# Kernel optimization log

Measured on AMD Instinct MI355X. Metric: run time of the kernel, lower is better.

## Reference

```python
import jax, jax.numpy as jnp
import numpy as np

N_NODES = 100000
N_EDGES = 1600000
IN_DIM, HID, OUT = 128, 64, 64
KERNEL = 5
PAD = (KERNEL - 1) // 2


def setup_inputs() -> dict:
    key = jax.random.key(0)
    ks = jax.random.split(key, 12)
    s = lambda fan_in: 1.0 / np.sqrt(fan_in)
    return {
        "x": jax.random.normal(ks[0], (N_NODES, IN_DIM), jnp.float32),
        "edge_index": jax.random.randint(ks[1], (2, N_EDGES), 0, N_NODES, jnp.int32),
        "W0": jax.random.normal(ks[2], (IN_DIM, HID), jnp.float32) * s(IN_DIM),
        "b0": jnp.zeros((HID,), jnp.float32),
        "W1": jax.random.normal(ks[3], (HID, HID), jnp.float32) * s(HID),
        "b1": jnp.zeros((HID,), jnp.float32),
        "W2": jax.random.normal(ks[4], (HID, OUT), jnp.float32) * s(HID),
        "b2": jnp.zeros((OUT,), jnp.float32),
        "Wp": jax.random.normal(ks[5], (OUT, 1), jnp.float32) * s(OUT),
        "bp": jnp.zeros((1,), jnp.float32),
        "conv1_w": jax.random.normal(ks[6], (OUT, OUT, KERNEL), jnp.float32) * s(OUT * KERNEL),
        "conv1_b": jnp.zeros((OUT,), jnp.float32),
        "conv2_w": jax.random.normal(ks[7], (OUT, OUT, KERNEL), jnp.float32) * s(OUT * KERNEL),
        "conv2_b": jnp.zeros((OUT,), jnp.float32),
        "lin_w": jax.random.normal(ks[8], (2 * OUT, OUT), jnp.float32) * s(2 * OUT),
        "lin_b": jnp.zeros((OUT,), jnp.float32),
    }


def gcn_conv(h, W, b, src, dst, n):
    """PyG GCNConv: x @ W, add self-loops, D^-1/2 (A+I) D^-1/2 aggregation, + bias."""
    h = h @ W  # [N, out]
    loop = jnp.arange(n, dtype=src.dtype)
    srcl = jnp.concatenate([src, loop])
    dstl = jnp.concatenate([dst, loop])
    deg = jax.ops.segment_sum(jnp.ones_like(dstl, dtype=h.dtype), dstl, num_segments=n)
    dinv = jnp.where(deg > 0, jax.lax.rsqrt(deg), 0.0)
    norm = dinv[srcl] * dinv[dstl]  # [E+N]
    out = jax.ops.segment_sum(h[srcl] * norm[:, None], dstl, num_segments=n)
    return out + b


def conv1d(x, w, b):
    # x: [1, C, N], w: [Cout, Cin, K]
    y = jax.lax.conv_general_dilated(x, w, window_strides=(1,), padding=[(PAD, PAD)],
                                     dimension_numbers=("NCH", "OIH", "NCH"))
    return y + b[None, :, None]


def reference(x, edge_index, W0, b0, W1, b1, W2, b2, Wp, bp,
              conv1_w, conv1_b, conv2_w, conv2_b, lin_w, lin_b):
    n = x.shape[0]
    src, dst = edge_index[0], edge_index[1]
    # eval mode: dropout layers are identity
    h = jax.nn.relu(gcn_conv(x, W0, b0, src, dst, n))
    h = jax.nn.relu(gcn_conv(h, W1, b1, src, dst, n))
    h1 = gcn_conv(h, W2, b2, src, dst, n)  # [N, OUT]
    g_score = h1 @ Wp + bp  # [N, 1]
    sorted_idx = jnp.argsort(g_score[:, 0])  # ascending, as torch.sort
    inverse_idx = jnp.argsort(sorted_idx)
    sorted_x = g_score[sorted_idx] * h1[sorted_idx]  # [N, OUT]
    sorted_x = sorted_x.T[None]  # [1, OUT, N]
    sorted_x = jax.nn.relu(conv1d(sorted_x, conv1_w, conv1_b))
    sorted_x = conv1d(sorted_x, conv2_w, conv2_b)
    sorted_x = sorted_x[0].T  # [N, OUT]
    h2 = sorted_x[inverse_idx]  # un-sort back to node order
    out = jnp.concatenate([h1, h2], axis=1) @ lin_w + lin_b  # [N, OUT]
    return out
```

## Files before the change

### kernel.cpp

```cpp
#include <hip/hip_runtime.h>

#define NN 100000
#define NE 1600000
#define NBUK 391
#define RBLK 98
#define NENT (256 * RBLK)
#define RSEG 25
#define BS_CHUNK 8192
#define NBS 196

__global__ void zero_bhist(int* bhist) {
    int i = blockIdx.x * blockDim.x + threadIdx.x;
    if (i < NBUK) bhist[i] = 0;
}

__global__ __launch_bounds__(256) void bucket_hist(const int* __restrict__ dst, int* __restrict__ bhist) {
    __shared__ int h[NBUK];
    int t = threadIdx.x;
    for (int b = t; b < NBUK; b += 256) h[b] = 0;
    __syncthreads();
    int base = blockIdx.x * BS_CHUNK;
    for (int i = t; i < BS_CHUNK; i += 256) {
        int e = base + i;
        if (e < NE) atomicAdd(&h[dst[e] >> 8], 1);
    }
    __syncthreads();
    for (int b = t; b < NBUK; b += 256)
        if (h[b]) atomicAdd(&bhist[b], h[b]);
}

__global__ __launch_bounds__(512) void bucket_scan(const int* __restrict__ bhist,
                                                   int* __restrict__ bbase, int* __restrict__ bcur) {
    __shared__ int tmp[512];
    int t = threadIdx.x;
    int v = (t < NBUK) ? bhist[t] : 0;
    tmp[t] = v; __syncthreads();
    for (int o = 1; o < 512; o <<= 1) {
        int add = (t >= o) ? tmp[t - o] : 0;
        __syncthreads();
        tmp[t] += add;
        __syncthreads();
    }
    int ex = tmp[t] - v;
    if (t < NBUK) { bbase[t] = ex; bcur[t] = ex; }
    if (t == NBUK - 1) bbase[NBUK] = ex + v;
}

__global__ __launch_bounds__(256) void bucket_scatter(const int* __restrict__ src,
                                                      const int* __restrict__ dst,
                                                      int* __restrict__ bcur,
                                                      unsigned* __restrict__ stage) {
    __shared__ int h[NBUK];
    int t = threadIdx.x;
    for (int b = t; b < NBUK; b += 256) h[b] = 0;
    __syncthreads();
    int base = blockIdx.x * BS_CHUNK;
    for (int i = t; i < BS_CHUNK; i += 256) {
        int e = base + i;
        if (e < NE) atomicAdd(&h[dst[e] >> 8], 1);
    }
    __syncthreads();
    for (int b = t; b < NBUK; b += 256) {
        int c = h[b];
        h[b] = c ? atomicAdd(&bcur[b], c) : 0;
    }
    __syncthreads();
    for (int i = t; i < BS_CHUNK; i += 256) {
        int e = base + i;
        if (e < NE) {
            int d = dst[e];
            int p = atomicAdd(&h[d >> 8], 1);
            stage[p] = ((unsigned)src[e] << 8) | (unsigned)(d & 255);
        }
    }
}

__global__ __launch_bounds__(256) void csr_place(const unsigned* __restrict__ stage,
                                                 const int* __restrict__ bbase,
                                                 int* __restrict__ csr,
                                                 int* __restrict__ counts,
                                                 int* __restrict__ offs,
                                                 float* __restrict__ dinv) {
    __shared__ int cnt[256];
    __shared__ int cursor[256];
    int b = blockIdx.x, t = threadIdx.x;
    int start = bbase[b], end = bbase[b + 1];
    cnt[t] = 0;
    __syncthreads();
    for (int idx = start + t; idx < end; idx += 256)
        atomicAdd(&cnt[stage[idx] & 255u], 1);
    __syncthreads();
    int c = cnt[t];
    __shared__ int tmp[256];
    tmp[t] = c; __syncthreads();
    for (int o = 1; o < 256; o <<= 1) {
        int add = (t >= o) ? tmp[t - o] : 0;
        __syncthreads();
        tmp[t] += add;
        __syncthreads();
    }
    int pos = start + tmp[t] - c;
    cursor[t] = pos;
    int node = b * 256 + t;
    if (node < NN) {
        offs[node] = pos;
        counts[node] = c;
        dinv[node] = rsqrtf((float)(c + 1));
    }
    __syncthreads();
    for (int idx = start + t; idx < end; idx += 256) {
        unsigned u = stage[idx];
        int p = atomicAdd(&cursor[u & 255u], 1);
        csr[p] = (int)(u >> 8);
    }
}

__device__ inline void swz_w(const float* __restrict__ W, float4* __restrict__ o, int idx) {
    int k4 = idx >> 6, co = idx & 63;
    o[idx] = make_float4(W[(4 * k4 + 0) * 64 + co], W[(4 * k4 + 1) * 64 + co],
                         W[(4 * k4 + 2) * 64 + co], W[(4 * k4 + 3) * 64 + co]);
}

__device__ inline void swz_c(const float* __restrict__ w, float4* __restrict__ o, int idx) {
    int co = idx & 63, j = (idx >> 6) & 15, k = idx >> 10;
    int b = co * 320 + k;
    o[idx] = make_float4(w[b + (4 * j + 0) * 5], w[b + (4 * j + 1) * 5],
                         w[b + (4 * j + 2) * 5], w[b + (4 * j + 3) * 5]);
}

__global__ void swizzle_all(const float* W0, const float* W1, const float* W2,
                            const float* lw, const float* c1w, const float* c2w,
                            float4* w0sw, float4* w1sw, float4* w2sw,
                            float4* linsw, float4* c1sw, float4* c2sw) {
    int idx = blockIdx.x * blockDim.x + threadIdx.x;
    if (idx < 2048)        swz_w(W0, w0sw, idx);
    else if (idx < 3072)   swz_w(W1, w1sw, idx - 2048);
    else if (idx < 4096)   swz_w(W2, w2sw, idx - 3072);
    else if (idx < 6144)   swz_w(lw, linsw, idx - 4096);
    else if (idx < 11264)  swz_c(c1w, c1sw, idx - 6144);
    else if (idx < 16384)  swz_c(c2w, c2sw, idx - 11264);
}

template <int K, bool RELU>
__global__ __launch_bounds__(256) void gemm64r(const float* __restrict__ X,
                                               const float4* __restrict__ Wsw,
                                               const float* __restrict__ dinv,
                                               float* __restrict__ Y, int n) {
    constexpr int KV = K / 4;
    constexpr int SH = (KV == 32) ? 5 : 4;
    __shared__ float4 xs[64][KV];
    int tid = threadIdx.x;
    int r0 = blockIdx.x * 64;
    for (int idx = tid; idx < 64 * KV; idx += 256) {
        int r = idx >> SH, k4 = idx & (KV - 1);
        int row = r0 + r;
        float4 v = make_float4(0.f, 0.f, 0.f, 0.f);
        if (row < n) v = *reinterpret_cast<const float4*>(X + (size_t)row * K + 4 * k4);
        if (RELU) {
            v.x = fmaxf(v.x, 0.f); v.y = fmaxf(v.y, 0.f);
            v.z = fmaxf(v.z, 0.f); v.w = fmaxf(v.w, 0.f);
        }
        xs[r][k4] = v;
    }
    __syncthreads();
    int co2 = tid & 31, rg = tid >> 5;
    int c0 = 2 * co2;
    float acc0[8], acc1[8];
#pragma unroll
    for (int i = 0; i < 8; i++) { acc0[i] = 0.f; acc1[i] = 0.f; }
    for (int k4 = 0; k4 < KV; k4++) {
        float4 wa = Wsw[k4 * 64 + c0];
        float4 wb = Wsw[k4 * 64 + c0 + 1];
#pragma unroll
        for (int i = 0; i < 8; i++) {
            float4 xv = xs[rg * 8 + i][k4];
            acc0[i] += xv.x * wa.x + xv.y * wa.y + xv.z * wa.z + xv.w * wa.w;
            acc1[i] += xv.x * wb.x + xv.y * wb.y + xv.z * wb.z + xv.w * wb.w;
        }
    }
#pragma unroll
    for (int i = 0; i < 8; i++) {
        int row = r0 + rg * 8 + i;
        if (row < n) {
            float dv = dinv[row];
            *reinterpret_cast<float2*>(Y + (size_t)row * 64 + c0) =
                make_float2(acc0[i] * dv, acc1[i] * dv);
        }
    }
}

template <int SCORE>
__global__ __launch_bounds__(256) void agg_pull(const float* __restrict__ H,
                                                const int* __restrict__ offs,
                                                const int* __restrict__ counts,
                                                const int* __restrict__ csr,
                                                const float* __restrict__ dinv,
                                                const float* __restrict__ bias,
                                                float* __restrict__ Y,
                                                const float* __restrict__ Wp,
                                                const float* __restrict__ bp,
                                                float* __restrict__ sc,
                                                unsigned* __restrict__ keys,
                                                int* __restrict__ vals) {
    int lane = threadIdx.x & 63;
    int node = blockIdx.x * 4 + (threadIdx.x >> 6);
    if (node >= NN) return;
    float dv = dinv[node];
    float acc = H[(size_t)node * 64 + lane];
    int off = offs[node], cnt = counts[node];
    int i = 0;
    for (; i + 7 < cnt; i += 8) {
        int p0 = csr[off + i];
        int p1 = csr[off + i + 1];
        int p2 = csr[off + i + 2];
        int p3 = csr[off + i + 3];
        int p4 = csr[off + i + 4];
        int p5 = csr[off + i + 5];
        int p6 = csr[off + i + 6];
        int p7 = csr[off + i + 7];
        float h0 = H[(size_t)p0 * 64 + lane];
        float h1 = H[(size_t)p1 * 64 + lane];
        float h2 = H[(size_t)p2 * 64 + lane];
        float h3 = H[(size_t)p3 * 64 + lane];
        float h4 = H[(size_t)p4 * 64 + lane];
        float h5 = H[(size_t)p5 * 64 + lane];
        float h6 = H[(size_t)p6 * 64 + lane];
        float h7 = H[(size_t)p7 * 64 + lane];
        acc += ((h0 + h1) + (h2 + h3)) + ((h4 + h5) + (h6 + h7));
    }
    for (; i < cnt; i++) {
        acc += H[(size_t)csr[off + i] * 64 + lane];
    }
    float o = acc * dv + bias[lane];
    Y[(size_t)node * 64 + lane] = o;
    if (SCORE) {
        float v = o * Wp[lane];
        for (int of = 32; of; of >>= 1) v += __shfl_down(v, of, 64);
        if (lane == 0) {
            float s = v + bp[0];
            sc[node] = s;
            unsigned u = __float_as_uint(s);
            u = (u & 0x80000000u) ? ~u : (u | 0x80000000u);
            keys[node] = u;
            vals[node] = node;
        }
    }
}

__global__ __launch_bounds__(256) void radix_hist(const unsigned* __restrict__ keys,
                                                  int* __restrict__ hist, int shift) {
    __shared__ int h[256];
    int t = threadIdx.x;
    h[t] = 0;
    __syncthreads();
    int base = blockIdx.x * 1024;
    for (int i = t; i < 1024; i += 256) {
        int idx = base + i;
        if (idx < NN) atomicAdd(&h[(keys[idx] >> shift) & 255], 1);
    }
    __syncthreads();
    hist[t * RBLK + blockIdx.x] = h[t];
}

__global__ __launch_bounds__(1024) void radix_scan(int* hist) {
    __shared__ int partial[1024];
    int t = threadIdx.x;
    int base = t * RSEG;
    int loc[RSEG];
    int s = 0;
#pragma unroll
    for (int i = 0; i < RSEG; i++) {
        int idx = base + i;
        int v = (idx < NENT) ? hist[idx] : 0;
        loc[i] = s;
        s += v;
    }
    partial[t] = s;
    __syncthreads();
    for (int o = 1; o < 1024; o <<= 1) {
        int add = (t >= o) ? partial[t - o] : 0;
        __syncthreads();
        partial[t] += add;
        __syncthreads();
    }
    int ex = partial[t] - s;
#pragma unroll
    for (int i = 0; i < RSEG; i++) {
        int idx = base + i;
        if (idx < NENT) hist[idx] = ex + loc[i];
    }
}

__global__ __launch_bounds__(256) void radix_scatter(const unsigned* __restrict__ keys_in,
                                                     const int* __restrict__ vals_in,
                                                     const int* __restrict__ hist,
                                                     unsigned* __restrict__ keys_out,
                                                     int* __restrict__ vals_out, int shift) {
    __shared__ int cursor[256];
    __shared__ int whist[4][256];
    __shared__ int wbase[4][256];
    int t = threadIdx.x, w = t >> 6, lane = t & 63;
    cursor[t] = hist[t * RBLK + blockIdx.x];
    __syncthreads();
    int base = blockIdx.x * 1024;
    for (int r = 0; r < 4; r++) {
        int idx = base + r * 256 + t;
        bool active = idx < NN;
        unsigned key = 0;
        int val = 0, d = -1;
        if (active) {
            key = keys_in[idx];
            val = vals_in[idx];
            d = (key >> shift) & 255;
        }
#pragma unroll
        for (int q = 0; q < 4; q++) whist[q][t] = 0;
        __syncthreads();
        unsigned long long m = __ballot(active);
#pragma unroll
        for (int b = 0; b < 8; b++) {
            unsigned long long bb = __ballot(active && ((d >> b) & 1));
            m &= ((d >> b) & 1) ? bb : ~bb;
        }
        unsigned long long below = ((unsigned long long)1 << lane) - 1;
        int rank_in_wave = __popcll(m & below);
        int cnt_in_wave = __popcll(m);
        if (active && rank_in_wave == 0) whist[w][d] = cnt_in_wave;
        __syncthreads();
        int c0 = whist[0][t], c1 = whist[1][t], c2 = whist[2][t], c3 = whist[3][t];
        wbase[0][t] = 0;
        wbase[1][t] = c0;
        wbase[2][t] = c0 + c1;
        wbase[3][t] = c0 + c1 + c2;
        __syncthreads();
        if (active) {
            int pos = cursor[d] + wbase[w][d] + rank_in_wave;
            keys_out[pos] = key;
            vals_out[pos] = val;
        }
        __syncthreads();
        cursor[t] += c0 + c1 + c2 + c3;
    }
}

template <bool GATHER>
__global__ __launch_bounds__(256) void conv1d_k(const float* __restrict__ X,
                                                const int* __restrict__ vals,
                                                const float* __restrict__ sc,
                                                const float4* __restrict__ cw,
                                                const float* __restrict__ bias,
                                                float* __restrict__ Y, int relu,
                                                int* __restrict__ inv) {
    __shared__ float4 xs[68][16];
    int tid = threadIdx.x;
    int r0 = blockIdx.x * 64;
    for (int idx = tid; idx < 68 * 16; idx += 256) {
        int r = idx >> 4, k4 = idx & 15;
        int row = r0 + r - 2;
        float4 v = make_float4(0.f, 0.f, 0.f, 0.f);
        if (row >= 0 && row < NN) {
            if (GATHER) {
                int vs = vals[row];
                float s = sc[vs];
                v = *reinterpret_cast<const float4*>(X + (size_t)vs * 64 + 4 * k4);
                v.x *= s; v.y *= s; v.z *= s; v.w *= s;
                if (k4 == 0) inv[vs] = row;
            } else {
                v = *reinterpret_cast<const float4*>(X + (size_t)row * 64 + 4 * k4);
            }
        }
        xs[r][k4] = v;
    }
    __syncthreads();
    int co2 = tid & 31, rg = tid >> 5;
    int c0 = 2 * co2;
    float acc0[8], acc1[8];
#pragma unroll
    for (int i = 0; i < 8; i++) { acc0[i] = 0.f; acc1[i] = 0.f; }
    for (int j = 0; j < 16; j++) {
        float4 xv[12];
#pragma unroll
        for (int t2 = 0; t2 < 12; t2++) xv[t2] = xs[rg * 8 + t2][j];
#pragma unroll
        for (int k = 0; k < 5; k++) {
            float4 wa = cw[(k * 16 + j) * 64 + c0];
            float4 wb = cw[(k * 16 + j) * 64 + c0 + 1];
#pragma unroll
            for (int i = 0; i < 8; i++) {
                float4 x4 = xv[i + k];
                acc0[i] += x4.x * wa.x + x4.y * wa.y + x4.z * wa.z + x4.w * wa.w;
                acc1[i] += x4.x * wb.x + x4.y * wb.y + x4.z * wb.z + x4.w * wb.w;
            }
        }
    }
    float b0v = bias[c0], b1v = bias[c0 + 1];
#pragma unroll
    for (int i = 0; i < 8; i++) {
        int row = r0 + rg * 8 + i;
        if (row < NN) {
            float o0 = acc0[i] + b0v, o1 = acc1[i] + b1v;
            if (relu) { o0 = fmaxf(o0, 0.f); o1 = fmaxf(o1, 0.f); }
            *reinterpret_cast<float2*>(Y + (size_t)row * 64 + c0) = make_float2(o0, o1);
        }
    }
}

__global__ __launch_bounds__(256) void final_k(const float* __restrict__ C,
                                               const float* __restrict__ H2,
                                               const int* __restrict__ inv,
                                               const float4* __restrict__ linsw,
                                               const float* __restrict__ lb,
                                               float* __restrict__ Yout) {
    __shared__ float4 xs[64][32];
    int tid = threadIdx.x;
    int r0 = blockIdx.x * 64;
    for (int idx = tid; idx < 64 * 32; idx += 256) {
        int r = idx >> 5, k4 = idx & 31;
        int row = r0 + r;
        float4 v = make_float4(0.f, 0.f, 0.f, 0.f);
        if (row < NN) {
            if (k4 < 16) v = *reinterpret_cast<const float4*>(C + (size_t)row * 64 + 4 * k4);
            else v = *reinterpret_cast<const float4*>(H2 + (size_t)inv[row] * 64 + 4 * (k4 - 16));
        }
        xs[r][k4] = v;
    }
    __syncthreads();
    int co2 = tid & 31, rg = tid >> 5;
    int c0 = 2 * co2;
    float acc0[8], acc1[8];
#pragma unroll
    for (int i = 0; i < 8; i++) { acc0[i] = 0.f; acc1[i] = 0.f; }
    for (int k4 = 0; k4 < 32; k4++) {
        float4 wa = linsw[k4 * 64 + c0];
        float4 wb = linsw[k4 * 64 + c0 + 1];
#pragma unroll
        for (int i = 0; i < 8; i++) {
            float4 xv = xs[rg * 8 + i][k4];
            acc0[i] += xv.x * wa.x + xv.y * wa.y + xv.z * wa.z + xv.w * wa.w;
            acc1[i] += xv.x * wb.x + xv.y * wb.y + xv.z * wb.z + xv.w * wb.w;
        }
    }
    float b0v = lb[c0], b1v = lb[c0 + 1];
#pragma unroll
    for (int i = 0; i < 8; i++) {
        int row = r0 + rg * 8 + i;
        if (row < NN)
            *reinterpret_cast<float2*>(Yout + (size_t)row * 64 + c0) =
                make_float2(acc0[i] + b0v, acc1[i] + b1v);
    }
}

extern "C" void kernel_launch(void* const* d_in, const int* in_sizes, int n_in,
                              void* d_out, int out_size, void* d_ws, size_t ws_size,
                              hipStream_t stream) {
    const float* x   = (const float*)d_in[0];
    const int*   ei  = (const int*)d_in[1];
    const float* W0  = (const float*)d_in[2];
    const float* b0  = (const float*)d_in[3];
    const float* W1  = (const float*)d_in[4];
    const float* b1  = (const float*)d_in[5];
    const float* W2  = (const float*)d_in[6];
    const float* b2  = (const float*)d_in[7];
    const float* Wp  = (const float*)d_in[8];
    const float* bp  = (const float*)d_in[9];
    const float* c1w = (const float*)d_in[10];
    const float* c1b = (const float*)d_in[11];
    const float* c2w = (const float*)d_in[12];
    const float* c2b = (const float*)d_in[13];
    const float* lw  = (const float*)d_in[14];
    const float* lb  = (const float*)d_in[15];
    const int* src = ei;
    const int* dst = ei + NE;

    const int NNP = 100352;
    float* A     = (float*)d_ws;
    float* B     = A + (size_t)NN * 64;
    float* dinv  = B + (size_t)NN * 64;
    float* score = dinv + NNP;
    unsigned* keys0 = (unsigned*)(score + NNP);
    int* vals0   = (int*)(keys0 + NNP);
    unsigned* keys1 = (unsigned*)(vals0 + NNP);
    int* vals1   = (int*)(keys1 + NNP);
    int* rhist   = vals1 + NNP;
    int* inv     = rhist + NENT;
    int* counts  = inv + NNP;
    int* offs    = counts + NNP;
    int* bhist   = offs + NNP;
    int* bbase   = bhist + 512;
    int* bcur    = bbase + 512;
    unsigned* stage = (unsigned*)(bcur + 512);
    int* csr     = (int*)(stage + NE);
    float4* w0sw  = (float4*)(csr + NE);
    float4* w1sw  = w0sw + 2048;
    float4* w2sw  = w1sw + 1024;
    float4* linsw = w2sw + 1024;
    float4* c1sw  = linsw + 2048;
    float4* c2sw  = c1sw + 5120;
    float* Cb = (float*)d_out;

    const int GR64 = (NN + 63) / 64;
    const int GN4 = (NN + 3) / 4;

    zero_bhist<<<2, 256, 0, stream>>>(bhist);
    bucket_hist<<<NBS, 256, 0, stream>>>(dst, bhist);
    bucket_scan<<<1, 512, 0, stream>>>(bhist, bbase, bcur);
    bucket_scatter<<<NBS, 256, 0, stream>>>(src, dst, bcur, stage);
    csr_place<<<NBUK, 256, 0, stream>>>(stage, bbase, csr, counts, offs, dinv);

    swizzle_all<<<64, 256, 0, stream>>>(W0, W1, W2, lw, c1w, c2w,
                                        w0sw, w1sw, w2sw, linsw, c1sw, c2sw);

    gemm64r<128, false><<<GR64, 256, 0, stream>>>(x, w0sw, dinv, A, NN);
    agg_pull<0><<<GN4, 256, 0, stream>>>(A, offs, counts, csr, dinv, b0, B,
                                         nullptr, nullptr, nullptr, nullptr, nullptr);
    gemm64r<64, true><<<GR64, 256, 0, stream>>>(B, w1sw, dinv, A, NN);
    agg_pull<0><<<GN4, 256, 0, stream>>>(A, offs, counts, csr, dinv, b1, B,
                                         nullptr, nullptr, nullptr, nullptr, nullptr);
    gemm64r<64, true><<<GR64, 256, 0, stream>>>(B, w2sw, dinv, A, NN);
    agg_pull<1><<<GN4, 256, 0, stream>>>(A, offs, counts, csr, dinv, b2, Cb,
                                         Wp, bp, score, keys0, vals0);

    radix_hist<<<RBLK, 256, 0, stream>>>(keys0, rhist, 0);
    radix_scan<<<1, 1024, 0, stream>>>(rhist);
    radix_scatter<<<RBLK, 256, 0, stream>>>(keys0, vals0, rhist, keys1, vals1, 0);
    radix_hist<<<RBLK, 256, 0, stream>>>(keys1, rhist, 8);
    radix_scan<<<1, 1024, 0, stream>>>(rhist);
    radix_scatter<<<RBLK, 256, 0, stream>>>(keys1, vals1, rhist, keys0, vals0, 8);
    radix_hist<<<RBLK, 256, 0, stream>>>(keys0, rhist, 16);
    radix_scan<<<1, 1024, 0, stream>>>(rhist);
    radix_scatter<<<RBLK, 256, 0, stream>>>(keys0, vals0, rhist, keys1, vals1, 16);
    radix_hist<<<RBLK, 256, 0, stream>>>(keys1, rhist, 24);
    radix_scan<<<1, 1024, 0, stream>>>(rhist);
    radix_scatter<<<RBLK, 256, 0, stream>>>(keys1, vals1, rhist, keys0, vals0, 24);

    conv1d_k<true><<<GR64, 256, 0, stream>>>(Cb, vals0, score, c1sw, c1b, B, 1, inv);
    conv1d_k<false><<<GR64, 256, 0, stream>>>(B, nullptr, nullptr, c2sw, c2b, A, 0, nullptr);

    final_k<<<GR64, 256, 0, stream>>>(Cb, A, inv, linsw, lb, (float*)d_out);
}
```

Before: 783.9 us.

## Fuse two conv1d passes into one kernel and halve row tiles to 32

The two sequential conv1d kernels become a single kernel. It gathers a 40-row halo tile, computes the first convolution plus ReLU into shared memory, then applies the second convolution from shared memory. This removes a global write and re-read of the intermediate activation and one launch, at the cost of recomputing halo rows. The GEMM, conv and final kernels also switch from 64-row/256-thread blocks to 32-row/128-thread blocks, which doubles the block count and may change occupancy. The fused conv holds more accumulators per thread and loads 13 float4 inputs, which adds register pressure.

```diff
diff --git a/kernel.cpp b/kernel.cpp
--- a/kernel.cpp
+++ b/kernel.cpp
@@ -142,16 +142,16 @@
 }
 
 template <int K, bool RELU>
-__global__ __launch_bounds__(256) void gemm64r(const float* __restrict__ X,
-                                               const float4* __restrict__ Wsw,
-                                               const float* __restrict__ dinv,
-                                               float* __restrict__ Y, int n) {
+__global__ __launch_bounds__(128) void gemm128t(const float* __restrict__ X,
+                                                const float4* __restrict__ Wsw,
+                                                const float* __restrict__ dinv,
+                                                float* __restrict__ Y, int n) {
     constexpr int KV = K / 4;
     constexpr int SH = (KV == 32) ? 5 : 4;
-    __shared__ float4 xs[64][KV];
+    __shared__ float4 xs[32][KV];
     int tid = threadIdx.x;
-    int r0 = blockIdx.x * 64;
-    for (int idx = tid; idx < 64 * KV; idx += 256) {
+    int r0 = blockIdx.x * 32;
+    for (int idx = tid; idx < 32 * KV; idx += 128) {
         int r = idx >> SH, k4 = idx & (KV - 1);
         int row = r0 + r;
         float4 v = make_float4(0.f, 0.f, 0.f, 0.f);
@@ -343,78 +343,112 @@
     }
 }
 
-template <bool GATHER>
-__global__ __launch_bounds__(256) void conv1d_k(const float* __restrict__ X,
-                                                const int* __restrict__ vals,
-                                                const float* __restrict__ sc,
-                                                const float4* __restrict__ cw,
-                                                const float* __restrict__ bias,
-                                                float* __restrict__ Y, int relu,
-                                                int* __restrict__ inv) {
-    __shared__ float4 xs[68][16];
+__global__ __launch_bounds__(128) void conv_fused(const float* __restrict__ X,
+                                                  const int* __restrict__ vals,
+                                                  const float* __restrict__ sc,
+                                                  const float4* __restrict__ cw1,
+                                                  const float* __restrict__ b1,
+                                                  const float4* __restrict__ cw2,
+                                                  const float* __restrict__ b2,
+                                                  float* __restrict__ Y,
+                                                  int* __restrict__ inv) {
+    __shared__ float4 xs[40][16];
+    __shared__ float y1[36][68];
     int tid = threadIdx.x;
-    int r0 = blockIdx.x * 64;
-    for (int idx = tid; idx < 68 * 16; idx += 256) {
+    int r0 = blockIdx.x * 32;
+    for (int idx = tid; idx < 40 * 16; idx += 128) {
         int r = idx >> 4, k4 = idx & 15;
-        int row = r0 + r - 2;
+        int row = r0 + r - 4;
         float4 v = make_float4(0.f, 0.f, 0.f, 0.f);
         if (row >= 0 && row < NN) {
-            if (GATHER) {
-                int vs = vals[row];
-                float s = sc[vs];
-                v = *reinterpret_cast<const float4*>(X + (size_t)vs * 64 + 4 * k4);
-                v.x *= s; v.y *= s; v.z *= s; v.w *= s;
-                if (k4 == 0) inv[vs] = row;
-            } else {
-                v = *reinterpret_cast<const float4*>(X + (size_t)row * 64 + 4 * k4);
-            }
+            int vs = vals[row];
+            float s = sc[vs];
+            v = *reinterpret_cast<const float4*>(X + (size_t)vs * 64 + 4 * k4);
+            v.x *= s; v.y *= s; v.z *= s; v.w *= s;
+            if (k4 == 0) inv[vs] = row;
         }
         xs[r][k4] = v;
     }
     __syncthreads();
     int co2 = tid & 31, rg = tid >> 5;
     int c0 = 2 * co2;
-    float acc0[8], acc1[8];
-#pragma unroll
-    for (int i = 0; i < 8; i++) { acc0[i] = 0.f; acc1[i] = 0.f; }
-    for (int j = 0; j < 16; j++) {
-        float4 xv[12];
-#pragma unroll
-        for (int t2 = 0; t2 < 12; t2++) xv[t2] = xs[rg * 8 + t2][j];
-#pragma unroll
-        for (int k = 0; k < 5; k++) {
-            float4 wa = cw[(k * 16 + j) * 64 + c0];
-            float4 wb = cw[(k * 16 + j) * 64 + c0 + 1];
-#pragma unroll
-            for (int i = 0; i < 8; i++) {
-                float4 x4 = xv[i + k];
-                acc0[i] += x4.x * wa.x + x4.y * wa.y + x4.z * wa.z + x4.w * wa.w;
-                acc1[i] += x4.x * wb.x + x4.y * wb.y + x4.z * wb.z + x4.w * wb.w;
+    {
+        float a0[9], a1[9];
+#pragma unroll
+        for (int i = 0; i < 9; i++) { a0[i] = 0.f; a1[i] = 0.f; }
+        for (int j = 0; j < 16; j++) {
+            float4 xv[13];
+#pragma unroll
+            for (int t2 = 0; t2 < 13; t2++) xv[t2] = xs[rg * 9 + t2][j];
+#pragma unroll
+            for (int k = 0; k < 5; k++) {
+                float4 wa = cw1[(k * 16 + j) * 64 + c0];
+                float4 wb = cw1[(k * 16 + j) * 64 + c0 + 1];
+#pragma unroll
+                for (int i = 0; i < 9; i++) {
+                    float4 x4 = xv[i + k];
+                    a0[i] += x4.x * wa.x + x4.y * wa.y + x4.z * wa.z + x4.w * wa.w;
+                    a1[i] += x4.x * wb.x + x4.y * wb.y + x4.z * wb.z + x4.w * wb.w;
+                }
             }
         }
-    }
-    float b0v = bias[c0], b1v = bias[c0 + 1];
-#pragma unroll
-    for (int i = 0; i < 8; i++) {
-        int row = r0 + rg * 8 + i;
-        if (row < NN) {
-            float o0 = acc0[i] + b0v, o1 = acc1[i] + b1v;
-            if (relu) { o0 = fmaxf(o0, 0.f); o1 = fmaxf(o1, 0.f); }
-            *reinterpret_cast<float2*>(Y + (size_t)row * 64 + c0) = make_float2(o0, o1);
-        }
-    }
-}
-
-__global__ __launch_bounds__(256) void final_k(const float* __restrict__ C,
+        float bv0 = b1[c0], bv1 = b1[c0 + 1];
+#pragma unroll
+        for (int i = 0; i < 9; i++) {
+            int yr = rg * 9 + i;
+            int g = r0 - 2 + yr;
+            float o0 = 0.f, o1 = 0.f;
+            if (g >= 0 && g < NN) {
+                o0 = fmaxf(a0[i] + bv0, 0.f);
+                o1 = fmaxf(a1[i] + bv1, 0.f);
+            }
+            y1[yr][c0] = o0;
+            y1[yr][c0 + 1] = o1;
+        }
+    }
+    __syncthreads();
+    {
+        float d0[8], d1[8];
+#pragma unroll
+        for (int i = 0; i < 8; i++) { d0[i] = 0.f; d1[i] = 0.f; }
+        for (int j = 0; j < 16; j++) {
+            float4 yv[12];
+#pragma unroll
+            for (int t2 = 0; t2 < 12; t2++)
+                yv[t2] = *reinterpret_cast<const float4*>(&y1[rg * 8 + t2][4 * j]);
+#pragma unroll
+            for (int k = 0; k < 5; k++) {
+                float4 wa = cw2[(k * 16 + j) * 64 + c0];
+                float4 wb = cw2[(k * 16 + j) * 64 + c0 + 1];
+#pragma unroll
+                for (int i = 0; i < 8; i++) {
+                    float4 x4 = yv[i + k];
+                    d0[i] += x4.x * wa.x + x4.y * wa.y + x4.z * wa.z + x4.w * wa.w;
+                    d1[i] += x4.x * wb.x + x4.y * wb.y + x4.z * wb.z + x4.w * wb.w;
+                }
+            }
+        }
+        float bv0 = b2[c0], bv1 = b2[c0 + 1];
+#pragma unroll
+        for (int i = 0; i < 8; i++) {
+            int row = r0 + rg * 8 + i;
+            if (row < NN)
+                *reinterpret_cast<float2*>(Y + (size_t)row * 64 + c0) =
+                    make_float2(d0[i] + bv0, d1[i] + bv1);
+        }
+    }
+}
+
+__global__ __launch_bounds__(128) void final_k(const float* __restrict__ C,
                                                const float* __restrict__ H2,
                                                const int* __restrict__ inv,
                                                const float4* __restrict__ linsw,
                                                const float* __restrict__ lb,
                                                float* __restrict__ Yout) {
-    __shared__ float4 xs[64][32];
+    __shared__ float4 xs[32][32];
     int tid = threadIdx.x;
-    int r0 = blockIdx.x * 64;
-    for (int idx = tid; idx < 64 * 32; idx += 256) {
+    int r0 = blockIdx.x * 32;
+    for (int idx = tid; idx < 32 * 32; idx += 128) {
         int r = idx >> 5, k4 = idx & 31;
         int row = r0 + r;
         float4 v = make_float4(0.f, 0.f, 0.f, 0.f);
@@ -498,7 +532,7 @@
     float4* c2sw  = c1sw + 5120;
     float* Cb = (float*)d_out;
 
-    const int GR64 = (NN + 63) / 64;
+    const int GR32 = (NN + 31) / 32;
     const int GN4 = (NN + 3) / 4;
 
     zero_bhist<<<2, 256, 0, stream>>>(bhist);
@@ -510,13 +544,13 @@
     swizzle_all<<<64, 256, 0, stream>>>(W0, W1, W2, lw, c1w, c2w,
                                         w0sw, w1sw, w2sw, linsw, c1sw, c2sw);
 
-    gemm64r<128, false><<<GR64, 256, 0, stream>>>(x, w0sw, dinv, A, NN);
+    gemm128t<128, false><<<GR32, 128, 0, stream>>>(x, w0sw, dinv, A, NN);
     agg_pull<0><<<GN4, 256, 0, stream>>>(A, offs, counts, csr, dinv, b0, B,
                                          nullptr, nullptr, nullptr, nullptr, nullptr);
-    gemm64r<64, true><<<GR64, 256, 0, stream>>>(B, w1sw, dinv, A, NN);
+    gemm128t<64, true><<<GR32, 128, 0, stream>>>(B, w1sw, dinv, A, NN);
     agg_pull<0><<<GN4, 256, 0, stream>>>(A, offs, counts, csr, dinv, b1, B,
                                          nullptr, nullptr, nullptr, nullptr, nullptr);
-    gemm64r<64, true><<<GR64, 256, 0, stream>>>(B, w2sw, dinv, A, NN);
+    gemm128t<64, true><<<GR32, 128, 0, stream>>>(B, w2sw, dinv, A, NN);
     agg_pull<1><<<GN4, 256, 0, stream>>>(A, offs, counts, csr, dinv, b2, Cb,
                                          Wp, bp, score, keys0, vals0);
 
@@ -533,8 +567,7 @@
     radix_scan<<<1, 1024, 0, stream>>>(rhist);
     radix_scatter<<<RBLK, 256, 0, stream>>>(keys1, vals1, rhist, keys0, vals0, 24);
 
-    conv1d_k<true><<<GR64, 256, 0, stream>>>(Cb, vals0, score, c1sw, c1b, B, 1, inv);
-    conv1d_k<false><<<GR64, 256, 0, stream>>>(B, nullptr, nullptr, c2sw, c2b, A, 0, nullptr);
-
-    final_k<<<GR64, 256, 0, stream>>>(Cb, A, inv, linsw, lb, (float*)d_out);
-}
+    conv_fused<<<GR32, 128, 0, stream>>>(Cb, vals0, score, c1sw, c1b, c2sw, c2b, A, inv);
+
+    final_k<<<GR32, 128, 0, stream>>>(Cb, A, inv, linsw, lb, (float*)d_out);
+}
```

Result: slower. 806.6 us (+2.9%).
